# Optimization experiments

Measured on AMD Instinct MI355X. Metric: run time of the kernel, lower is better.

Reference implementation:

```python
import jax, jax.numpy as jnp
import numpy as np

B, S, HID = 2, 2048, 1024
H, D = 16, 64  # head_dim = HID // H
MAXPOS = 2048


def setup_inputs() -> dict:
    key = jax.random.key(0)
    ks = jax.random.split(key, 9)
    s = 0.02
    return {
        "hidden_states": jax.random.normal(ks[0], (B, S, HID), jnp.float32),
        "attention_mask": jnp.zeros((B, 1, 1, S), jnp.float32),
        "Wq": jax.random.normal(ks[1], (HID, HID), jnp.float32) * s,
        "bq": jnp.zeros((HID,), jnp.float32),
        "Wk": jax.random.normal(ks[2], (HID, HID), jnp.float32) * s,
        "bk": jnp.zeros((HID,), jnp.float32),
        "Wv": jax.random.normal(ks[3], (HID, HID), jnp.float32) * s,
        "bv": jnp.zeros((HID,), jnp.float32),
        "dist_emb": jax.random.normal(ks[4], (2 * MAXPOS - 1, D), jnp.float32) * s,
    }


def reference(hidden_states, attention_mask, Wq, bq, Wk, bk, Wv, bv, dist_emb):
    b, s, _ = hidden_states.shape

    def heads(x):  # [B,S,HID] -> [B,H,S,D]
        return x.reshape(b, s, H, D).transpose(0, 2, 1, 3)

    q = heads(hidden_states @ Wq.T + bq)
    k = heads(hidden_states @ Wk.T + bk)
    v = heads(hidden_states @ Wv.T + bv)

    # raw scores [B,H,L,R]
    scores = jnp.einsum("bhld,bhrd->bhlr", q, k)

    # relative_key_query position bias
    pos_l = jnp.arange(s)[:, None]
    pos_r = jnp.arange(s)[None, :]
    distance = pos_l - pos_r + (MAXPOS - 1)  # [L,R]
    pos_emb = dist_emb[distance]  # [L,R,D]
    rel_q = jnp.einsum("bhld,lrd->bhlr", q, pos_emb)
    rel_k = jnp.einsum("bhrd,lrd->bhlr", k, pos_emb)
    scores = scores + rel_q + rel_k

    scores = scores / jnp.sqrt(jnp.asarray(D, scores.dtype))
    scores = scores + attention_mask  # additive mask broadcast [B,1,1,R]

    probs = jax.nn.softmax(scores, axis=-1)  # dropout p=0 -> identity
    ctx = jnp.einsum("bhlr,bhrd->bhld", probs, v)  # [B,H,L,D]
    ctx = ctx.transpose(0, 2, 1, 3).reshape(b, s, H * D)
    return ctx
```

## Files before the change

kernel.cpp:

```cpp
#include <hip/hip_runtime.h>

typedef __bf16 bf16_t;
typedef __bf16 bf16x8 __attribute__((ext_vector_type(8)));
typedef __bf16 bf16x4v __attribute__((ext_vector_type(4)));
typedef float floatx4 __attribute__((ext_vector_type(4)));

#define MFMA16(a, b, c) __builtin_amdgcn_mfma_f32_16x16x32_bf16((a), (b), (c), 0, 0, 0)

constexpr int S_ = 2048;
constexpr int HID_ = 1024;
constexpr int HH = 16;
constexpr int DD = 64;

__global__ __launch_bounds__(256) void cvt_all_kernel(
    const float* __restrict__ h, const float* __restrict__ wq, const float* __restrict__ wk,
    const float* __restrict__ wv, const float* __restrict__ de, bf16_t* __restrict__ hb,
    bf16_t* __restrict__ wb, bf16_t* __restrict__ eb) {
  int v = blockIdx.x * 256 + threadIdx.x;
  if (v >= 1900528) return;
  const float* src;
  bf16_t* dst;
  int off;
  if (v < 1048576) {
    src = h; dst = hb; off = v;
  } else if (v < 1310720) {
    src = wq; dst = wb; off = v - 1048576;
  } else if (v < 1572864) {
    src = wk; dst = wb + 1048576; off = v - 1310720;
  } else if (v < 1835008) {
    src = wv; dst = wb + 2097152; off = v - 1572864;
  } else {
    src = de; dst = eb; off = v - 1835008;
  }
  float4 f = *(const float4*)(src + (size_t)off * 4);
  bf16x4v p = {(bf16_t)f.x, (bf16_t)f.y, (bf16_t)f.z, (bf16_t)f.w};
  *(bf16x4v*)(dst + (size_t)off * 4) = p;
}

__global__ __launch_bounds__(256) void cvt_e_kernel(const float* __restrict__ src,
                                                    bf16_t* __restrict__ dst, int n) {
  int i = blockIdx.x * 256 + threadIdx.x;
  if (i < n) dst[i] = (bf16_t)src[i];
}

__global__ __launch_bounds__(256) void qkv_gemm2_kernel(
    const bf16_t* __restrict__ hb, const bf16_t* __restrict__ wb,
    const float* __restrict__ bq, const float* __restrict__ bk, const float* __restrict__ bv,
    bf16_t* __restrict__ qb, bf16_t* __restrict__ kb, bf16_t* __restrict__ vb) {
  __shared__ alignas(16) bf16_t As[128][72];
  __shared__ alignas(16) bf16_t Bs[128][72];
  const int z = blockIdx.z;
  const bf16_t* W = wb + (size_t)z * HID_ * HID_;
  const float* bias = (z == 0) ? bq : (z == 1) ? bk : bv;
  bf16_t* out = (z == 0) ? qb : (z == 1) ? kb : vb;
  const int transposed = (z == 2);

  const int tid = threadIdx.x;
  const int lane = tid & 63, wid = tid >> 6;
  const int l15 = lane & 15, quad = lane >> 4;
  const int m0 = blockIdx.x * 128, n0 = blockIdx.y * 128;
  const int wm = (wid >> 1) * 64, wn = (wid & 1) * 64;
  floatx4 acc[4][4] = {};
  const int srow = tid >> 1, sch = (tid & 1) * 32;
  const bf16_t* aptr = hb + (size_t)(m0 + srow) * HID_ + sch;
  const bf16_t* bptr = W + (size_t)(n0 + srow) * HID_ + sch;

  for (int k0 = 0; k0 < HID_; k0 += 64) {
    __syncthreads();
#pragma unroll
    for (int j = 0; j < 4; ++j) {
      *(bf16x8*)&As[srow][sch + j * 8] = *(const bf16x8*)(aptr + k0 + j * 8);
      *(bf16x8*)&Bs[srow][sch + j * 8] = *(const bf16x8*)(bptr + k0 + j * 8);
    }
    __syncthreads();
    bf16x8 af[4][2], bfv[4][2];
#pragma unroll
    for (int t = 0; t < 4; ++t)
#pragma unroll
      for (int kh = 0; kh < 2; ++kh) {
        af[t][kh] = *(const bf16x8*)&As[wm + t * 16 + l15][kh * 32 + quad * 8];
        bfv[t][kh] = *(const bf16x8*)&Bs[wn + t * 16 + l15][kh * 32 + quad * 8];
      }
#pragma unroll
    for (int mt = 0; mt < 4; ++mt)
#pragma unroll
      for (int nt = 0; nt < 4; ++nt) {
        acc[mt][nt] = MFMA16(af[mt][0], bfv[nt][0], acc[mt][nt]);
        acc[mt][nt] = MFMA16(af[mt][1], bfv[nt][1], acc[mt][nt]);
      }
  }

#pragma unroll
  for (int nt = 0; nt < 4; ++nt) {
    int o = n0 + wn + nt * 16 + l15;
    float bvs = bias[o];
    int h = o >> 6, d = o & 63;
#pragma unroll
    for (int mt = 0; mt < 4; ++mt) {
      int sb = m0 + wm + mt * 16 + quad * 4;
      int b = sb >> 11, s = sb & 2047;
      if (!transposed) {
        bf16_t* dst = out + (((size_t)(b * HH + h) * S_ + s) * DD + d);
#pragma unroll
        for (int i = 0; i < 4; ++i) dst[(size_t)i * DD] = (bf16_t)(acc[mt][nt][i] + bvs);
      } else {
        bf16_t* dst = out + (((size_t)(b * HH + h) * DD + d) * S_ + s);
        bf16x4v pk = {(bf16_t)(acc[mt][nt][0] + bvs), (bf16_t)(acc[mt][nt][1] + bvs),
                      (bf16_t)(acc[mt][nt][2] + bvs), (bf16_t)(acc[mt][nt][3] + bvs)};
        *(bf16x4v*)dst = pk;
      }
    }
  }
}

__global__ __launch_bounds__(256) void qkv_gemm_kernel(
    const float* __restrict__ X, const float* __restrict__ W,
    const float* __restrict__ bias, bf16_t* __restrict__ out, int transposed) {
  __shared__ alignas(16) bf16_t As[128][40];
  __shared__ alignas(16) bf16_t Bs[128][40];
  const int tid = threadIdx.x;
  const int lane = tid & 63, wid = tid >> 6;
  const int l15 = lane & 15, quad = lane >> 4;
  const int m0 = blockIdx.x * 128, n0 = blockIdx.y * 128;
  const int wm = (wid >> 1) * 64, wn = (wid & 1) * 64;
  floatx4 acc[4][4] = {};
  const int srow = tid >> 1, scol = (tid & 1) * 16;
  const float* aptr = X + (size_t)(m0 + srow) * HID_ + scol;
  const float* bptr = W + (size_t)(n0 + srow) * HID_ + scol;

  for (int k0 = 0; k0 < HID_; k0 += 32) {
    __syncthreads();
    {
      const float4* a4 = (const float4*)(aptr + k0);
      float4 f0 = a4[0], f1 = a4[1], f2 = a4[2], f3 = a4[3];
      bf16x4v p0 = {(bf16_t)f0.x, (bf16_t)f0.y, (bf16_t)f0.z, (bf16_t)f0.w};
      bf16x4v p1 = {(bf16_t)f1.x, (bf16_t)f1.y, (bf16_t)f1.z, (bf16_t)f1.w};
      bf16x4v p2 = {(bf16_t)f2.x, (bf16_t)f2.y, (bf16_t)f2.z, (bf16_t)f2.w};
      bf16x4v p3 = {(bf16_t)f3.x, (bf16_t)f3.y, (bf16_t)f3.z, (bf16_t)f3.w};
      *(bf16x4v*)&As[srow][scol + 0] = p0;
      *(bf16x4v*)&As[srow][scol + 4] = p1;
      *(bf16x4v*)&As[srow][scol + 8] = p2;
      *(bf16x4v*)&As[srow][scol + 12] = p3;
      const float4* b4 = (const float4*)(bptr + k0);
      float4 g0 = b4[0], g1 = b4[1], g2 = b4[2], g3 = b4[3];
      bf16x4v q0 = {(bf16_t)g0.x, (bf16_t)g0.y, (bf16_t)g0.z, (bf16_t)g0.w};
      bf16x4v q1 = {(bf16_t)g1.x, (bf16_t)g1.y, (bf16_t)g1.z, (bf16_t)g1.w};
      bf16x4v q2 = {(bf16_t)g2.x, (bf16_t)g2.y, (bf16_t)g2.z, (bf16_t)g2.w};
      bf16x4v q3 = {(bf16_t)g3.x, (bf16_t)g3.y, (bf16_t)g3.z, (bf16_t)g3.w};
      *(bf16x4v*)&Bs[srow][scol + 0] = q0;
      *(bf16x4v*)&Bs[srow][scol + 4] = q1;
      *(bf16x4v*)&Bs[srow][scol + 8] = q2;
      *(bf16x4v*)&Bs[srow][scol + 12] = q3;
    }
    __syncthreads();
    bf16x8 af[4], bfv[4];
#pragma unroll
    for (int t = 0; t < 4; ++t) af[t] = *(const bf16x8*)&As[wm + t * 16 + l15][quad * 8];
#pragma unroll
    for (int t = 0; t < 4; ++t) bfv[t] = *(const bf16x8*)&Bs[wn + t * 16 + l15][quad * 8];
#pragma unroll
    for (int mt = 0; mt < 4; ++mt)
#pragma unroll
      for (int nt = 0; nt < 4; ++nt)
        acc[mt][nt] = MFMA16(af[mt], bfv[nt], acc[mt][nt]);
  }

#pragma unroll
  for (int nt = 0; nt < 4; ++nt) {
    int o = n0 + wn + nt * 16 + l15;
    float bv = bias[o];
    int h = o >> 6, d = o & 63;
#pragma unroll
    for (int mt = 0; mt < 4; ++mt) {
      int sb = m0 + wm + mt * 16 + quad * 4;
      int b = sb >> 11, s = sb & 2047;
      if (!transposed) {
        bf16_t* dst = out + (((size_t)(b * HH + h) * S_ + s) * DD + d);
#pragma unroll
        for (int i = 0; i < 4; ++i) dst[(size_t)i * DD] = (bf16_t)(acc[mt][nt][i] + bv);
      } else {
        bf16_t* dst = out + (((size_t)(b * HH + h) * DD + d) * S_ + s);
        bf16x4v pk = {(bf16_t)(acc[mt][nt][0] + bv), (bf16_t)(acc[mt][nt][1] + bv),
                      (bf16_t)(acc[mt][nt][2] + bv), (bf16_t)(acc[mt][nt][3] + bv)};
        *(bf16x4v*)dst = pk;
      }
    }
  }
}

__global__ __launch_bounds__(256, 3) void attn7_kernel(
    const bf16_t* __restrict__ Q, const bf16_t* __restrict__ K,
    const bf16_t* __restrict__ Vt, const bf16_t* __restrict__ E,
    const float* __restrict__ mask, float* __restrict__ out) {
  __shared__ alignas(16) bf16_t Er[128 * 64];
  __shared__ alignas(16) bf16_t Vs[64 * 64];
  __shared__ alignas(16) bf16_t PX[65 * 72];
  __shared__ alignas(16) bf16_t X1t[64][132];
  __shared__ float lsumS[4][64];

  const int tid = threadIdx.x;
  const int lane = tid & 63, wid = tid >> 6;
  const int l15 = lane & 15, quad = lane >> 4;
  const int bh = blockIdx.x & 31, lblk = blockIdx.x >> 5;
  const int l0 = lblk * 64;
  const bf16_t* Qb = Q + (size_t)bh * S_ * DD;
  const bf16_t* Kb = K + (size_t)bh * S_ * DD;
  const bf16_t* Vb = Vt + (size_t)bh * DD * S_;
  const float* maskb = mask + (size_t)(bh >> 4) * S_;

  bf16x8 qB[4][2];
#pragma unroll
  for (int ct = 0; ct < 4; ++ct) {
    const bf16_t* qp = Qb + (size_t)(l0 + ct * 16 + l15) * DD + quad * 8;
    qB[ct][0] = *(const bf16x8*)qp;
    qB[ct][1] = *(const bf16x8*)(qp + 32);
  }

  {
    int rr = tid >> 2, c0 = (tid & 3) * 2;
    int grow = l0 + 2048 + rr;
    if (grow > 4094) grow = 4094;
    const bf16_t* ep = E + (size_t)grow * DD + c0 * 8;
    bf16x8 e0 = *(const bf16x8*)ep;
    bf16x8 e1 = *(const bf16x8*)(ep + 8);
    int slot = (l0 + 2048 + rr) & 127, sw = rr & 7;
    *(bf16x8*)&Er[slot * 64 + (((c0 + 0) ^ sw) << 3)] = e0;
    *(bf16x8*)&Er[slot * 64 + (((c0 + 1) ^ sw) << 3)] = e1;
  }
  __syncthreads();

#pragma unroll
  for (int wt = 0; wt < 4; ++wt) {
    int sr = (l0 + 2048 + wt * 16 + l15) & 127;
    int sw = l15 & 7;
    bf16x8 e0 = *(const bf16x8*)&Er[sr * 64 + ((quad ^ sw) << 3)];
    bf16x8 e1 = *(const bf16x8*)&Er[sr * 64 + (((4 + quad) ^ sw) << 3)];
    floatx4 t1 = {};
    t1 = MFMA16(qB[wid][0], e0, t1);
    t1 = MFMA16(qB[wid][1], e1, t1);
    const int wl = wt * 16 + l15;
#pragma unroll
    for (int i = 0; i < 4; ++i) {
      int ll = wid * 16 + quad * 4 + i;
      int r = ll - wl - 1;
      int col = (r >= 0) ? r : (128 + i);
      X1t[ll][col] = (bf16_t)t1[i];
    }
  }

  floatx4 Oacc[4] = {};
  float lsum[4] = {0.f, 0.f, 0.f, 0.f};
  const float SCL = 0.125f * 1.44269504f;

  for (int r0 = 0; r0 < S_; r0 += 64) {
    const int A = l0 - r0 + 1984;
    {
      int rr = tid >> 2, c0 = (tid & 3) * 2;
      const bf16_t* ep = E + (size_t)(A + rr) * DD + c0 * 8;
      bf16x8 e0 = *(const bf16x8*)ep;
      bf16x8 e1 = *(const bf16x8*)(ep + 8);
      int slot = (A + rr) & 127, sw = rr & 7;
      *(bf16x8*)&Er[slot * 64 + (((c0 + 0) ^ sw) << 3)] = e0;
      *(bf16x8*)&Er[slot * 64 + (((c0 + 1) ^ sw) << 3)] = e1;
    }
    const bf16_t* kp = Kb + (size_t)(r0 + wid * 16 + l15) * DD + quad * 8;
    bf16x8 kf0 = *(const bf16x8*)kp;
    bf16x8 kf1 = *(const bf16x8*)(kp + 32);
    float4 m4 = *(const float4*)(maskb + r0 + wid * 16 + quad * 4);
    float m8[4] = {m4.x * 8.f, m4.y * 8.f, m4.z * 8.f, m4.w * 8.f};
    __syncthreads();

#pragma unroll
    for (int wt = 0; wt < 8; ++wt) {
      const bool needT1 = (wt < 4);
      const bool needT2 = (wt + wid >= 3) && (wt + wid <= 7);
      if (!(needT1 || needT2)) continue;
      int sr = (A + wt * 16 + l15) & 127;
      int sw = l15 & 7;
      bf16x8 e0 = *(const bf16x8*)&Er[sr * 64 + ((quad ^ sw) << 3)];
      bf16x8 e1 = *(const bf16x8*)&Er[sr * 64 + (((4 + quad) ^ sw) << 3)];
      const int wl = wt * 16 + l15;
      if (needT2) {
        floatx4 t2 = {};
        t2 = MFMA16(kf0, e0, t2);
        t2 = MFMA16(kf1, e1, t2);
#pragma unroll
        for (int i = 0; i < 4; ++i) {
          int rl = wid * 16 + quad * 4 + i;
          int ll = rl + wl - 63;
          PX[(((unsigned)ll < 64u) ? ll : 64) * 72 + rl] = (bf16_t)(t2[i] + m8[i]);
        }
      }
      if (needT1) {
        floatx4 t1 = {};
        t1 = MFMA16(qB[wid][0], e0, t1);
        t1 = MFMA16(qB[wid][1], e1, t1);
#pragma unroll
        for (int i = 0; i < 4; ++i) {
          int ll = wid * 16 + quad * 4 + i;
          int rc = (r0 + 63 + ll - wl) & 127;
          X1t[ll][rc] = (bf16_t)t1[i];
        }
      }
    }
    {
      int row = tid >> 2, c0 = (tid & 3) * 2;
      const bf16_t* vp = Vb + (size_t)row * S_ + r0 + c0 * 8;
      bf16x8 v0 = *(const bf16x8*)vp;
      bf16x8 v1 = *(const bf16x8*)(vp + 8);
      int h7 = row & 7;
      *(bf16x8*)&Vs[row * 64 + (((c0 + 0) ^ h7) << 3)] = v0;
      *(bf16x8*)&Vs[row * 64 + (((c0 + 1) ^ h7) << 3)] = v1;
    }
    __syncthreads();

    const int xc = (r0 + wid * 16 + quad * 4) & 127;
#pragma unroll
    for (int ct = 0; ct < 4; ++ct) {
      floatx4 s = {};
      s = MFMA16(kf0, qB[ct][0], s);
      s = MFMA16(kf1, qB[ct][1], s);
      bf16x4v x1 = *(const bf16x4v*)&X1t[ct * 16 + l15][xc];
      bf16_t* px = &PX[(ct * 16 + l15) * 72 + wid * 16 + quad * 4];
      bf16x4v x2 = *(const bf16x4v*)px;
      bf16x4v pk;
#pragma unroll
      for (int i = 0; i < 4; ++i) {
        float sv = s[i] + (float)x1[i] + (float)x2[i];
        float p = __builtin_amdgcn_exp2f(sv * SCL);
        lsum[ct] += p;
        pk[i] = (bf16_t)p;
      }
      *(bf16x4v*)px = pk;
    }
    __syncthreads();

    {
      const int prow = wid * 16 + l15;
      bf16x8 pf0 = *(const bf16x8*)&PX[prow * 72 + quad * 8];
      bf16x8 pf1 = *(const bf16x8*)&PX[prow * 72 + 32 + quad * 8];
#pragma unroll
      for (int dt = 0; dt < 4; ++dt) {
        int vrow = dt * 16 + l15;
        int vh = vrow & 7;
        bf16x8 v0 = *(const bf16x8*)&Vs[vrow * 64 + ((quad ^ vh) << 3)];
        bf16x8 v1 = *(const bf16x8*)&Vs[vrow * 64 + (((4 + quad) ^ vh) << 3)];
        Oacc[dt] = MFMA16(v0, pf0, Oacc[dt]);
        Oacc[dt] = MFMA16(v1, pf1, Oacc[dt]);
      }
    }
  }

#pragma unroll
  for (int ct = 0; ct < 4; ++ct) {
    lsum[ct] += __shfl_xor(lsum[ct], 16);
    lsum[ct] += __shfl_xor(lsum[ct], 32);
  }
  __syncthreads();
  if (quad == 0) {
#pragma unroll
    for (int ct = 0; ct < 4; ++ct) lsumS[wid][ct * 16 + l15] = lsum[ct];
  }
  __syncthreads();
  const int lidx = wid * 16 + l15;
  float tot = lsumS[0][lidx] + lsumS[1][lidx] + lsumS[2][lidx] + lsumS[3][lidx];
  float inv = 1.f / tot;
  const int b = bh >> 4, h = bh & 15;
  float* dst = out + (size_t)(b * S_ + l0 + lidx) * HID_ + h * DD + quad * 4;
#pragma unroll
  for (int dt = 0; dt < 4; ++dt) {
    float4 o = {Oacc[dt][0] * inv, Oacc[dt][1] * inv, Oacc[dt][2] * inv, Oacc[dt][3] * inv};
    *(float4*)(dst + dt * 16) = o;
  }
}

extern "C" void kernel_launch(void* const* d_in, const int* in_sizes, int n_in,
                              void* d_out, int out_size, void* d_ws, size_t ws_size,
                              hipStream_t stream) {
  const float* hidden = (const float*)d_in[0];
  const float* amask = (const float*)d_in[1];
  const float* Wq = (const float*)d_in[2];
  const float* bq = (const float*)d_in[3];
  const float* Wk = (const float*)d_in[4];
  const float* bk = (const float*)d_in[5];
  const float* Wv = (const float*)d_in[6];
  const float* bv = (const float*)d_in[7];
  const float* de = (const float*)d_in[8];
  float* outp = (float*)d_out;
  char* ws = (char*)d_ws;
  const size_t MB = 1024 * 1024;
  bf16_t* qb = (bf16_t*)(ws);
  bf16_t* kb = (bf16_t*)(ws + 8 * MB);
  bf16_t* vb = (bf16_t*)(ws + 16 * MB);
  bf16_t* eb = (bf16_t*)(ws + 24 * MB);
  bf16_t* hb = (bf16_t*)(ws + 25 * MB);
  bf16_t* wb = (bf16_t*)(ws + 33 * MB);

  if (ws_size >= 39 * MB) {
    cvt_all_kernel<<<dim3(7424), 256, 0, stream>>>(hidden, Wq, Wk, Wv, de, hb, wb, eb);
    qkv_gemm2_kernel<<<dim3(32, 8, 3), 256, 0, stream>>>(hb, wb, bq, bk, bv, qb, kb, vb);
  } else {
    cvt_e_kernel<<<dim3(1024), 256, 0, stream>>>(de, eb, 4095 * 64);
    dim3 g(32, 8);
    qkv_gemm_kernel<<<g, 256, 0, stream>>>(hidden, Wq, bq, qb, 0);
    qkv_gemm_kernel<<<g, 256, 0, stream>>>(hidden, Wk, bk, kb, 0);
    qkv_gemm_kernel<<<g, 256, 0, stream>>>(hidden, Wv, bv, vb, 1);
  }
  attn7_kernel<<<dim3(1024), 256, 0, stream>>>(qb, kb, vb, eb, amask, outp);
}
```

Before: 302.3 us.

## Use async global-to-LDS copies in QKV GEMM, fold softmax scale into Q, swizzle PX

```diff
diff --git a/kernel.cpp b/kernel.cpp
--- a/kernel.cpp
+++ b/kernel.cpp
@@ -11,6 +11,13 @@
 constexpr int HID_ = 1024;
 constexpr int HH = 16;
 constexpr int DD = 64;
+constexpr float ALPHA = 0.125f * 1.44269504f;
+constexpr float LOG2E = 1.44269504f;
+
+__device__ __forceinline__ void async_copy16(const bf16_t* g, bf16_t* l) {
+  __builtin_amdgcn_global_load_lds((const __attribute__((address_space(1))) unsigned int*)g,
+                                   (__attribute__((address_space(3))) unsigned int*)l, 16, 0, 0);
+}
 
 __global__ __launch_bounds__(256) void cvt_all_kernel(
     const float* __restrict__ h, const float* __restrict__ wq, const float* __restrict__ wk,
@@ -43,34 +50,31 @@
   if (i < n) dst[i] = (bf16_t)src[i];
 }
 
-__global__ __launch_bounds__(256) void qkv_gemm2_kernel(
+__global__ __launch_bounds__(256) void qkv_gemm3_kernel(
     const bf16_t* __restrict__ hb, const bf16_t* __restrict__ wb,
     const float* __restrict__ bq, const float* __restrict__ bk, const float* __restrict__ bv,
     bf16_t* __restrict__ qb, bf16_t* __restrict__ kb, bf16_t* __restrict__ vb) {
-  __shared__ alignas(16) bf16_t As[128][72];
-  __shared__ alignas(16) bf16_t Bs[128][72];
-  const int z = blockIdx.z;
-  const bf16_t* W = wb + (size_t)z * HID_ * HID_;
-  const float* bias = (z == 0) ? bq : (z == 1) ? bk : bv;
-  bf16_t* out = (z == 0) ? qb : (z == 1) ? kb : vb;
-  const int transposed = (z == 2);
-
+  __shared__ alignas(16) bf16_t As[128 * 64];
+  __shared__ alignas(16) bf16_t Bs[128 * 64];
   const int tid = threadIdx.x;
   const int lane = tid & 63, wid = tid >> 6;
   const int l15 = lane & 15, quad = lane >> 4;
   const int m0 = blockIdx.x * 128, n0 = blockIdx.y * 128;
   const int wm = (wid >> 1) * 64, wn = (wid & 1) * 64;
   floatx4 acc[4][4] = {};
-  const int srow = tid >> 1, sch = (tid & 1) * 32;
-  const bf16_t* aptr = hb + (size_t)(m0 + srow) * HID_ + sch;
-  const bf16_t* bptr = W + (size_t)(n0 + srow) * HID_ + sch;
+  const int srow = wid * 8 + (lane >> 3);
+  const int scol = (lane & 7) * 8;
+  const bf16_t* aptr = hb + (size_t)(m0 + srow) * HID_ + scol;
+  const bf16_t* bptr = wb + (size_t)(n0 + srow) * HID_ + scol;
+  bf16_t* As_w = As + (size_t)(wid * 8) * 64;
+  bf16_t* Bs_w = Bs + (size_t)(wid * 8) * 64;
 
   for (int k0 = 0; k0 < HID_; k0 += 64) {
     __syncthreads();
 #pragma unroll
-    for (int j = 0; j < 4; ++j) {
-      *(bf16x8*)&As[srow][sch + j * 8] = *(const bf16x8*)(aptr + k0 + j * 8);
-      *(bf16x8*)&Bs[srow][sch + j * 8] = *(const bf16x8*)(bptr + k0 + j * 8);
+    for (int p = 0; p < 4; ++p) {
+      async_copy16(aptr + k0 + (size_t)p * 32 * HID_, As_w + p * 32 * 64);
+      async_copy16(bptr + k0 + (size_t)p * 32 * HID_, Bs_w + p * 32 * 64);
     }
     __syncthreads();
     bf16x8 af[4][2], bfv[4][2];
@@ -78,8 +82,8 @@
     for (int t = 0; t < 4; ++t)
 #pragma unroll
       for (int kh = 0; kh < 2; ++kh) {
-        af[t][kh] = *(const bf16x8*)&As[wm + t * 16 + l15][kh * 32 + quad * 8];
-        bfv[t][kh] = *(const bf16x8*)&Bs[wn + t * 16 + l15][kh * 32 + quad * 8];
+        af[t][kh] = *(const bf16x8*)&As[(wm + t * 16 + l15) * 64 + kh * 32 + quad * 8];
+        bfv[t][kh] = *(const bf16x8*)&Bs[(wn + t * 16 + l15) * 64 + kh * 32 + quad * 8];
       }
 #pragma unroll
     for (int mt = 0; mt < 4; ++mt)
@@ -90,19 +94,23 @@
       }
   }
 
+  const int z = n0 >> 10;
+  const float* bias = (z == 0) ? bq : (z == 1) ? bk : bv;
+  bf16_t* out = (z == 0) ? qb : (z == 1) ? kb : vb;
+  const float scl = (z == 0) ? ALPHA : 1.0f;
 #pragma unroll
   for (int nt = 0; nt < 4; ++nt) {
-    int o = n0 + wn + nt * 16 + l15;
-    float bvs = bias[o];
-    int h = o >> 6, d = o & 63;
+    int oo = (n0 & 1023) + wn + nt * 16 + l15;
+    float bvs = bias[oo];
+    int h = oo >> 6, d = oo & 63;
 #pragma unroll
     for (int mt = 0; mt < 4; ++mt) {
       int sb = m0 + wm + mt * 16 + quad * 4;
       int b = sb >> 11, s = sb & 2047;
-      if (!transposed) {
+      if (z != 2) {
         bf16_t* dst = out + (((size_t)(b * HH + h) * S_ + s) * DD + d);
 #pragma unroll
-        for (int i = 0; i < 4; ++i) dst[(size_t)i * DD] = (bf16_t)(acc[mt][nt][i] + bvs);
+        for (int i = 0; i < 4; ++i) dst[(size_t)i * DD] = (bf16_t)((acc[mt][nt][i] + bvs) * scl);
       } else {
         bf16_t* dst = out + (((size_t)(b * HH + h) * DD + d) * S_ + s);
         bf16x4v pk = {(bf16_t)(acc[mt][nt][0] + bvs), (bf16_t)(acc[mt][nt][1] + bvs),
@@ -115,7 +123,7 @@
 
 __global__ __launch_bounds__(256) void qkv_gemm_kernel(
     const float* __restrict__ X, const float* __restrict__ W,
-    const float* __restrict__ bias, bf16_t* __restrict__ out, int transposed) {
+    const float* __restrict__ bias, bf16_t* __restrict__ out, int transposed, float scl) {
   __shared__ alignas(16) bf16_t As[128][40];
   __shared__ alignas(16) bf16_t Bs[128][40];
   const int tid = threadIdx.x;
@@ -177,7 +185,7 @@
       if (!transposed) {
         bf16_t* dst = out + (((size_t)(b * HH + h) * S_ + s) * DD + d);
 #pragma unroll
-        for (int i = 0; i < 4; ++i) dst[(size_t)i * DD] = (bf16_t)(acc[mt][nt][i] + bv);
+        for (int i = 0; i < 4; ++i) dst[(size_t)i * DD] = (bf16_t)((acc[mt][nt][i] + bv) * scl);
       } else {
         bf16_t* dst = out + (((size_t)(b * HH + h) * DD + d) * S_ + s);
         bf16x4v pk = {(bf16_t)(acc[mt][nt][0] + bv), (bf16_t)(acc[mt][nt][1] + bv),
@@ -188,14 +196,14 @@
   }
 }
 
-__global__ __launch_bounds__(256, 3) void attn7_kernel(
+__global__ __launch_bounds__(256, 3) void attn8_kernel(
     const bf16_t* __restrict__ Q, const bf16_t* __restrict__ K,
     const bf16_t* __restrict__ Vt, const bf16_t* __restrict__ E,
     const float* __restrict__ mask, float* __restrict__ out) {
   __shared__ alignas(16) bf16_t Er[128 * 64];
   __shared__ alignas(16) bf16_t Vs[64 * 64];
-  __shared__ alignas(16) bf16_t PX[65 * 72];
-  __shared__ alignas(16) bf16_t X1t[64][132];
+  __shared__ alignas(16) bf16_t PX[65 * 64];
+  __shared__ alignas(16) bf16_t X1t[64][134];
   __shared__ float lsumS[4][64];
 
   const int tid = threadIdx.x;
@@ -250,7 +258,6 @@
 
   floatx4 Oacc[4] = {};
   float lsum[4] = {0.f, 0.f, 0.f, 0.f};
-  const float SCL = 0.125f * 1.44269504f;
 
   for (int r0 = 0; r0 < S_; r0 += 64) {
     const int A = l0 - r0 + 1984;
@@ -267,7 +274,7 @@
     bf16x8 kf0 = *(const bf16x8*)kp;
     bf16x8 kf1 = *(const bf16x8*)(kp + 32);
     float4 m4 = *(const float4*)(maskb + r0 + wid * 16 + quad * 4);
-    float m8[4] = {m4.x * 8.f, m4.y * 8.f, m4.z * 8.f, m4.w * 8.f};
+    float mlg[4] = {m4.x * LOG2E, m4.y * LOG2E, m4.z * LOG2E, m4.w * LOG2E};
     __syncthreads();
 
 #pragma unroll
@@ -288,7 +295,9 @@
         for (int i = 0; i < 4; ++i) {
           int rl = wid * 16 + quad * 4 + i;
           int ll = rl + wl - 63;
-          PX[(((unsigned)ll < 64u) ? ll : 64) * 72 + rl] = (bf16_t)(t2[i] + m8[i]);
+          int row = ((unsigned)ll < 64u) ? ll : 64;
+          int col = (((rl >> 3) ^ (row & 7)) << 3) + (rl & 7);
+          PX[row * 64 + col] = (bf16_t)(t2[i] * ALPHA + mlg[i]);
         }
       }
       if (needT1) {
@@ -315,19 +324,21 @@
     __syncthreads();
 
     const int xc = (r0 + wid * 16 + quad * 4) & 127;
+    const int pc = wid * 2 + (quad >> 1);
 #pragma unroll
     for (int ct = 0; ct < 4; ++ct) {
       floatx4 s = {};
       s = MFMA16(kf0, qB[ct][0], s);
       s = MFMA16(kf1, qB[ct][1], s);
       bf16x4v x1 = *(const bf16x4v*)&X1t[ct * 16 + l15][xc];
-      bf16_t* px = &PX[(ct * 16 + l15) * 72 + wid * 16 + quad * 4];
+      const int row = ct * 16 + l15;
+      bf16_t* px = &PX[row * 64 + (((pc ^ (row & 7)) << 3) + ((quad & 1) << 2))];
       bf16x4v x2 = *(const bf16x4v*)px;
       bf16x4v pk;
 #pragma unroll
       for (int i = 0; i < 4; ++i) {
         float sv = s[i] + (float)x1[i] + (float)x2[i];
-        float p = __builtin_amdgcn_exp2f(sv * SCL);
+        float p = __builtin_amdgcn_exp2f(sv);
         lsum[ct] += p;
         pk[i] = (bf16_t)p;
       }
@@ -337,8 +348,9 @@
 
     {
       const int prow = wid * 16 + l15;
-      bf16x8 pf0 = *(const bf16x8*)&PX[prow * 72 + quad * 8];
-      bf16x8 pf1 = *(const bf16x8*)&PX[prow * 72 + 32 + quad * 8];
+      const int ph = prow & 7;
+      bf16x8 pf0 = *(const bf16x8*)&PX[prow * 64 + ((quad ^ ph) << 3)];
+      bf16x8 pf1 = *(const bf16x8*)&PX[prow * 64 + (((4 + quad) ^ ph) << 3)];
 #pragma unroll
       for (int dt = 0; dt < 4; ++dt) {
         int vrow = dt * 16 + l15;
@@ -398,13 +410,13 @@
 
   if (ws_size >= 39 * MB) {
     cvt_all_kernel<<<dim3(7424), 256, 0, stream>>>(hidden, Wq, Wk, Wv, de, hb, wb, eb);
-    qkv_gemm2_kernel<<<dim3(32, 8, 3), 256, 0, stream>>>(hb, wb, bq, bk, bv, qb, kb, vb);
+    qkv_gemm3_kernel<<<dim3(32, 24), 256, 0, stream>>>(hb, wb, bq, bk, bv, qb, kb, vb);
   } else {
     cvt_e_kernel<<<dim3(1024), 256, 0, stream>>>(de, eb, 4095 * 64);
     dim3 g(32, 8);
-    qkv_gemm_kernel<<<g, 256, 0, stream>>>(hidden, Wq, bq, qb, 0);
-    qkv_gemm_kernel<<<g, 256, 0, stream>>>(hidden, Wk, bk, kb, 0);
-    qkv_gemm_kernel<<<g, 256, 0, stream>>>(hidden, Wv, bv, vb, 1);
-  }
-  attn7_kernel<<<dim3(1024), 256, 0, stream>>>(qb, kb, vb, eb, amask, outp);
-}
+    qkv_gemm_kernel<<<g, 256, 0, stream>>>(hidden, Wq, bq, qb, 0, ALPHA);
+    qkv_gemm_kernel<<<g, 256, 0, stream>>>(hidden, Wk, bk, kb, 0, 1.0f);
+    qkv_gemm_kernel<<<g, 256, 0, stream>>>(hidden, Wv, bv, vb, 1, 1.0f);
+  }
+  attn8_kernel<<<dim3(1024), 256, 0, stream>>>(qb, kb, vb, eb, amask, outp);
+}
```

Result: no change. 303.8 us (+0.5%).
